# Performance work log

Measured on AMD Instinct MI355X. Metric: run time of the kernel, lower is better.

## Reference

```python
import jax, jax.numpy as jnp
import numpy as np

N_NODES = 50000
N_EDGES = 800000
HIDDEN = 128
EPS = 1e-5


def _layernorm(x, g, b):
    m = jnp.mean(x, axis=-1, keepdims=True)
    v = jnp.var(x, axis=-1, keepdims=True)
    return (x - m) / jnp.sqrt(v + EPS) * g + b


def _batchnorm(x, g, b):
    # training-mode BatchNorm1d: stats over the node (batch) axis, biased var
    m = jnp.mean(x, axis=0, keepdims=True)
    v = jnp.var(x, axis=0, keepdims=True)
    return (x - m) / jnp.sqrt(v + EPS) * g + b


def _instnorm(x):
    # torch InstanceNorm1d on a 2D [N,C] input: unbatched (C,L) view ->
    # normalize each row over the feature axis, no affine params
    m = jnp.mean(x, axis=-1, keepdims=True)
    v = jnp.var(x, axis=-1, keepdims=True)
    return (x - m) / jnp.sqrt(v + EPS)


def _gcn_conv(x, W, b, row, col, norm, n):
    # PyG GCNConv: out[col] += norm * (x @ W)[row]; + bias
    xw = x @ W
    msgs = xw[row] * norm[:, None]          # [E+N, H]
    out = jax.ops.segment_sum(msgs, col, num_segments=n)
    return out + b


def setup_inputs() -> dict:
    key = jax.random.key(0)
    ks = jax.random.split(key, 12)
    H = HIDDEN
    x = jax.random.normal(ks[0], (N_NODES, 2), dtype=jnp.float32)
    edge_index = jax.random.randint(ks[1], (2, N_EDGES), 0, N_NODES, dtype=jnp.int64)

    def lin(k, fan_in, shape):
        bound = 1.0 / np.sqrt(fan_in)
        return jax.random.uniform(k, shape, jnp.float32, -bound, bound)

    inp = {
        "x": x,
        "edge_index": edge_index,
        "coord_W": lin(ks[2], 2, (2, H)),
        "coord_b": lin(ks[3], 2, (H,)),
        "ln_g": jnp.ones((H,), jnp.float32),
        "ln_b": jnp.zeros((H,), jnp.float32),
        "bn_g": jnp.ones((H,), jnp.float32),
        "bn_b": jnp.zeros((H,), jnp.float32),
        "W1": lin(ks[4], H, (H, H)),
        "b1": jnp.zeros((H,), jnp.float32),
        "W2": lin(ks[5], H, (H, H)),
        "b2": jnp.zeros((H,), jnp.float32),
        "W3": lin(ks[6], H, (H, H)),
        "b3": jnp.zeros((H,), jnp.float32),
        "fc1_W": lin(ks[7], H, (H, 32)),
        "fc1_b": lin(ks[8], H, (32,)),
        "fc2_W": lin(ks[9], 32, (32, 2)),
        "fc2_b": lin(ks[10], 32, (2,)),
    }
    return inp


def reference(x, edge_index, coord_W, coord_b, ln_g, ln_b, bn_g, bn_b,
              W1, b1, W2, b2, W3, b3, fc1_W, fc1_b, fc2_W, fc2_b):
    n = x.shape[0]
    loop = jnp.arange(n, dtype=edge_index.dtype)
    row = jnp.concatenate([edge_index[0], loop])
    col = jnp.concatenate([edge_index[1], loop])
    deg = jax.ops.segment_sum(jnp.ones_like(col, dtype=x.dtype), col, num_segments=n)
    dinv = 1.0 / jnp.sqrt(deg)              # deg >= 1 thanks to self-loops
    norm = dinv[row] * dinv[col]

    h = jax.nn.relu(x @ coord_W + coord_b)
    h = _layernorm(h, ln_g, ln_b)

    for W, b in ((W1, b1), (W2, b2), (W3, b3)):
        identity = h
        h = jax.nn.relu(_gcn_conv(h, W, b, row, col, norm, n))
        h = _batchnorm(h, bn_g, bn_b)
        h = _instnorm(h + identity)

    h = jax.nn.relu(h @ fc1_W + fc1_b)
    return jnp.tanh(h @ fc2_W + fc2_b)
```

## Files before the change

### kernel.cpp

```cpp
#include <hip/hip_runtime.h>
#include <hip/hip_bf16.h>
#include <hip/hip_fp16.h>
#include <stdint.h>

#define NN 50000
#define NE 800000
#define HD 128
#define EPSN 1e-5f
#define CAP 1152000

typedef __hip_bfloat16 bf16;
typedef __attribute__((ext_vector_type(8))) _Float16 half8;
typedef __attribute__((ext_vector_type(4))) float f32x4;

__device__ __forceinline__ float us2f(unsigned short u) { return __uint_as_float((uint32_t)u << 16); }
__device__ __forceinline__ ushort f2us(float f) {
    bf16 b = __float2bfloat16(f);
    return *reinterpret_cast<ushort*>(&b);
}
__device__ __forceinline__ ushort f2h(float f) {
    __half h = __float2half(f);
    return *reinterpret_cast<ushort*>(&h);
}
__device__ __forceinline__ float h2f(ushort u) {
    __half h = *reinterpret_cast<__half*>(&u);
    return __half2float(h);
}

__device__ __forceinline__ void cvt8(float4 v, float* o) {
    uint32_t a = __float_as_uint(v.x), b = __float_as_uint(v.y);
    uint32_t c = __float_as_uint(v.z), d = __float_as_uint(v.w);
    o[0] = h2f((ushort)(a & 0xffff)); o[1] = h2f((ushort)(a >> 16));
    o[2] = h2f((ushort)(b & 0xffff)); o[3] = h2f((ushort)(b >> 16));
    o[4] = h2f((ushort)(c & 0xffff)); o[5] = h2f((ushort)(c >> 16));
    o[6] = h2f((ushort)(d & 0xffff)); o[7] = h2f((ushort)(d >> 16));
}

#define O_X    0
#define O_CW   100000
#define O_CB   100256
#define O_LNG  100384
#define O_LNB  100512
#define O_BNG  100640
#define O_BNB  100768
#define O_W1   100896
#define O_B1   117280
#define O_W2   117408
#define O_B2   133792
#define O_W3   133920
#define O_B3   150304
#define O_F1W  150432
#define O_F1B  154528
#define O_F2W  154560
#define O_F2B  154624
#define O_TOT  154626

struct Ptrs { const void* p[17]; };

__device__ const int SEG_OFF[18] = {O_X, O_CW, O_CB, O_LNG, O_LNB, O_BNG, O_BNB,
                                    O_W1, O_B1, O_W2, O_B2, O_W3, O_B3,
                                    O_F1W, O_F1B, O_F2W, O_F2B, O_TOT};

__device__ __forceinline__ int eidx(const int* __restrict__ ei, int isL, int which, int e) {
    size_t base = (size_t)which * NE + e;
    return isL ? ei[2 * base] : ei[base];
}

__global__ void k_detect(const int* __restrict__ ei, const ushort* __restrict__ cw,
                         int* __restrict__ flags) {
    int t = threadIdx.x;
    int v = ei[2 * t + 1] | ei[1000000 + 2 * t + 1];
    int bad = 0;
    if (t < 128) {
        float val = us2f(cw[2 * t]);
        bad = !(fabsf(val) <= 1.0f);
    }
    for (int o = 32; o; o >>= 1) { v |= __shfl_xor(v, o); bad |= __shfl_xor(bad, o); }
    __shared__ int sv[4], sb[4];
    if ((t & 63) == 0) { sv[t >> 6] = v; sb[t >> 6] = bad; }
    __syncthreads();
    if (t == 0) {
        flags[0] = ((sv[0] | sv[1] | sv[2] | sv[3]) == 0) ? 1 : 0;
        flags[1] = ((sb[0] | sb[1] | sb[2] | sb[3]) == 0) ? 1 : 0;
    }
}

__global__ void k_conv(Ptrs ptrs, const int* __restrict__ flags, float* __restrict__ cp,
                       _Float16* __restrict__ wt, int* __restrict__ degR,
                       float* __restrict__ stats, int* __restrict__ cursor,
                       ushort* __restrict__ t0h) {
    int i = blockIdx.x * 256 + threadIdx.x;
    int isBf = flags[1];
    if (i < O_TOT) {
        int s = 0;
        while (i >= SEG_OFF[s + 1]) s++;
        int local = i - SEG_OFF[s];
        const void* src = ptrs.p[s];
        cp[i] = isBf ? us2f(((const ushort*)src)[local]) : ((const float*)src)[local];
    }
    if (i < 3 * HD * HD) {
        int mat = i >> 14, idx = i & (HD * HD - 1);
        int k = idx >> 7, n = idx & 127;
        const void* src = ptrs.p[7 + 2 * mat];
        int local = k * HD + n;
        float v = isBf ? us2f(((const ushort*)src)[local]) : ((const float*)src)[local];
        wt[mat * HD * HD + n * HD + k] = (_Float16)v;
    }
    if (i < 8 * NN) degR[i] = (i < NN) ? 1 : 0;
    if (i < 12288) stats[i] = 0.f;
    if (i < HD) t0h[(size_t)NN * HD + i] = 0;
    if (i == 0) *cursor = 0;
}

__global__ void k_deg(const int* __restrict__ ei, const int* __restrict__ flags,
                      int* __restrict__ degR) {
    int e = blockIdx.x * 256 + threadIdx.x;
    if (e < NE) atomicAdd(&degR[(blockIdx.x & 7) * NN + eidx(ei, flags[0], 1, e)], 1);
}

__global__ void k_fill(const int* __restrict__ ei, const int* __restrict__ flags,
                       int* __restrict__ curA8, int* __restrict__ srw) {
    int e = blockIdx.x * 256 + threadIdx.x;
    if (e >= NE) return;
    int isL = flags[0];
    int r = eidx(ei, isL, 0, e);
    int c = eidx(ei, isL, 1, e);
    int p = atomicAdd(&curA8[(blockIdx.x & 7) * NN + c], 1);
    srw[p] = r << 4;
}


__global__ void k_embed(const float* __restrict__ cp, ushort* __restrict__ h,
                        const int* __restrict__ degR, float* __restrict__ dinv,
                        int* __restrict__ startA, int* __restrict__ curA8,
                        int* __restrict__ cursor, int* __restrict__ srw,
                        int* __restrict__ degO) {
    int gi = blockIdx.x * 256 + threadIdx.x;
    if (gi < NN) {
        int c[8];
        int d = 0;
#pragma unroll
        for (int r = 0; r < 8; r++) { c[r] = degR[r * NN + gi]; d += c[r]; }
        c[0] -= 1;
        degO[gi] = d;
        dinv[gi] = rsqrtf((float)d);
        int cnt = d - 1;
        int cpad = (cnt + 7) & ~7;
        int s = atomicAdd(cursor, cpad);
        startA[gi] = s;
        int off = 0;
#pragma unroll
        for (int r = 0; r < 8; r++) { curA8[r * NN + gi] = s + off; off += c[r]; }
        for (int p = s + cnt; p < s + cpad; p++) srw[p] = NN << 4;
    }
    int node = gi >> 6;
    int lane = threadIdx.x & 63;
    if (node >= NN) return;
    const float* X = cp + O_X;
    const float* CW = cp + O_CW;
    const float* CB = cp + O_CB;
    const float* LG = cp + O_LNG;
    const float* LB = cp + O_LNB;
    float x0 = X[node * 2], x1 = X[node * 2 + 1];
    int f0 = lane, f1 = lane + 64;
    float v0 = fmaxf(0.f, x0 * CW[f0] + x1 * CW[HD + f0] + CB[f0]);
    float v1 = fmaxf(0.f, x0 * CW[f1] + x1 * CW[HD + f1] + CB[f1]);
    float s = v0 + v1, q = v0 * v0 + v1 * v1;
    for (int o = 32; o; o >>= 1) { s += __shfl_xor(s, o); q += __shfl_xor(q, o); }
    float m = s * (1.f / HD);
    float var = q * (1.f / HD) - m * m;
    float r = rsqrtf(var + EPSN);
    h[(size_t)node * HD + f0] = f2h((v0 - m) * r * LG[f0] + LB[f0]);
    h[(size_t)node * HD + f1] = f2h((v1 - m) * r * LG[f1] + LB[f1]);
}


__device__ __forceinline__ void mfma_tile(const _Float16* hl, const _Float16* __restrict__ wt,
                                          const float* __restrict__ dinv,
                                          ushort* __restrict__ t0h, int nodeBase, int t) {
    int w = t >> 6, l = t & 63;
    int m16 = l & 15;
    int kg = l >> 4;
    int node0 = w * 16;
    half8 a[4];
#pragma unroll
    for (int kc = 0; kc < 4; kc++) {
        int nd = node0 + m16;
        int c16 = kc * 4 + kg;
        int chunk = nd * 16 + (c16 ^ (nd & 7));
        a[kc] = *(const half8*)(hl + chunk * 8);
    }
    f32x4 acc[8];
#pragma unroll
    for (int nt = 0; nt < 8; nt++) acc[nt] = (f32x4){0.f, 0.f, 0.f, 0.f};
#pragma unroll
    for (int nt = 0; nt < 8; nt++) {
        const half8* bp = (const half8*)(wt + (size_t)(nt * 16 + m16) * HD);
#pragma unroll
        for (int kc = 0; kc < 4; kc++) {
            acc[nt] = __builtin_amdgcn_mfma_f32_16x16x32_f16(a[kc], bp[kc * 4 + kg],
                                                             acc[nt], 0, 0, 0);
        }
    }
    int ndb = nodeBase + node0 + kg * 4;
#pragma unroll
    for (int rr = 0; rr < 4; rr++) {
        int nd = ndb + rr;
        if (nd < NN) {
            float dv = dinv[nd];
#pragma unroll
            for (int nt = 0; nt < 8; nt++) {
                t0h[(size_t)nd * HD + nt * 16 + m16] = f2h(acc[nt][rr] * dv);
            }
        }
    }
}


__global__ __launch_bounds__(256) void k_gemm(const ushort* __restrict__ h,
                                              const _Float16* __restrict__ wt,
                                              const float* __restrict__ dinv,
                                              ushort* __restrict__ t0h) {
    __shared__ _Float16 hl[64 * HD];
    int t = threadIdx.x;
    int nodeBase = blockIdx.x * 64;
    const uint4* h4 = (const uint4*)h;
#pragma unroll
    for (int r = 0; r < 4; r++) {
        int cid = r * 256 + t;
        int node = cid >> 4;
        int c16 = cid & 15;
        int n = nodeBase + node;
        uint4 v = make_uint4(0u, 0u, 0u, 0u);
        if (n < NN) v = h4[(size_t)n * 16 + c16];
        int chunk = node * 16 + (c16 ^ (node & 7));
        *(uint4*)(hl + chunk * 8) = v;
    }
    __syncthreads();
    mfma_tile(hl, wt, dinv, t0h, nodeBase, t);
}


__global__ __launch_bounds__(256) void k_gemm_fused(const float* __restrict__ agg,
                                                    const float* __restrict__ stats,
                                                    const float* __restrict__ bias,
                                                    const float* __restrict__ bng,
                                                    const float* __restrict__ bnb,
                                                    ushort* __restrict__ h,
                                                    const _Float16* __restrict__ wt,
                                                    const float* __restrict__ dinv,
                                                    ushort* __restrict__ t0h) {
    __shared__ _Float16 hl[64 * HD];
    __shared__ float scL[HD], shL[HD], bL[HD];
    int t = threadIdx.x;
    if (t < 128) {
        const float invN = 1.f / NN;
        float sv = 0.f, qv = 0.f;
#pragma unroll
        for (int r = 0; r < 16; r++) { sv += stats[r * 256 + t]; qv += stats[r * 256 + 128 + t]; }
        float m = sv * invN;
        float v = qv * invN - m * m;
        float sc = bng[t] * rsqrtf(v + EPSN);
        scL[t] = sc;
        shL[t] = bnb[t] - m * sc;
        bL[t] = bias[t];
    }
    __syncthreads();
    int nodeBase = blockIdx.x * 64;
    const float4* a4 = (const float4*)agg;
    const ushort4* h4r = (const ushort4*)h;
    ushort4* h4w = (ushort4*)h;
#pragma unroll
    for (int r = 0; r < 8; r++) {
        int idx = r * 256 + t;
        int node = idx >> 5;
        int c4 = idx & 31;
        int n = nodeBase + node;
        float4 u = make_float4(0.f, 0.f, 0.f, 0.f);
        if (n < NN) {
            float4 av = a4[(size_t)n * 32 + c4];
            ushort4 hv = h4r[(size_t)n * 32 + c4];
            int f = c4 * 4;
            float y0 = fmaxf(0.f, av.x + bL[f]);
            float y1 = fmaxf(0.f, av.y + bL[f + 1]);
            float y2 = fmaxf(0.f, av.z + bL[f + 2]);
            float y3 = fmaxf(0.f, av.w + bL[f + 3]);
            u.x = y0 * scL[f]     + shL[f]     + h2f(hv.x);
            u.y = y1 * scL[f + 1] + shL[f + 1] + h2f(hv.y);
            u.z = y2 * scL[f + 2] + shL[f + 2] + h2f(hv.z);
            u.w = y3 * scL[f + 3] + shL[f + 3] + h2f(hv.w);
        }
        float s = u.x + u.y + u.z + u.w;
        float q = u.x * u.x + u.y * u.y + u.z * u.z + u.w * u.w;
        for (int o = 16; o; o >>= 1) { s += __shfl_xor(s, o); q += __shfl_xor(q, o); }
        float m = s * (1.f / HD);
        float var = q * (1.f / HD) - m * m;
        float rr = rsqrtf(var + EPSN);
        u.x = (u.x - m) * rr; u.y = (u.y - m) * rr;
        u.z = (u.z - m) * rr; u.w = (u.w - m) * rr;
        ushort4 pk;
        pk.x = f2h(u.x); pk.y = f2h(u.y); pk.z = f2h(u.z); pk.w = f2h(u.w);
        if (n < NN) h4w[(size_t)n * 32 + c4] = pk;
        int chunk = node * 16 + ((c4 >> 1) ^ (node & 7));
        *(ushort4*)((char*)hl + chunk * 16 + (c4 & 1) * 8) = pk;
    }
    __syncthreads();
    mfma_tile(hl, wt, dinv, t0h, nodeBase, t);
}


__global__ __launch_bounds__(256) void k_agg(const ushort* __restrict__ t0h,
                                             const int* __restrict__ srw,
                                             const int* __restrict__ startA,
                                             const int* __restrict__ deg,
                                             const float* __restrict__ dinv,
                                             const float* __restrict__ bias,
                                             float* __restrict__ agg,
                                             float* __restrict__ stats) {
    int t = threadIdx.x;
    int w = t >> 6;
    int l = t & 63;
    int g = l >> 4;
    int k = l & 15;
    int l32 = l & 31;
    const float4* t04 = (const float4*)t0h;
    float4* agg4 = (float4*)agg;
    float bs[8];
    {
        const float4* b4 = (const float4*)bias;
        float4 u0 = b4[2 * k], u1 = b4[2 * k + 1];
        bs[0] = u0.x; bs[1] = u0.y; bs[2] = u0.z; bs[3] = u0.w;
        bs[4] = u1.x; bs[5] = u1.y; bs[6] = u1.z; bs[7] = u1.w;
    }
    float rs1[8], rs2[8];
#pragma unroll
    for (int m = 0; m < 8; m++) { rs1[m] = 0.f; rs2[m] = 0.f; }
    int stride = gridDim.x * 4;
    int i = blockIdx.x * 4 + w;
    int s = 0, nb = 0;
    float di = 0.f;
    if (i < NN) {
        s = startA[i];
        nb = (deg[i] - 1 + 7) & ~7;
        di = dinv[i];
    }
    while (i < NN) {
        float4 sv = t04[(size_t)i * 16 + k];
        int ex = 0;
        if (l32 < nb) ex = srw[s + l32];
        int nb4 = nb >> 2;
        float4 gg[8];
#define GATH(b) { int rv = __shfl(ex, 4 * (b) + g); \
                  gg[b] = t04[(size_t)(uint32_t)rv + k]; }
        if (nb4 > 0) { GATH(0) GATH(1) }
        if (nb4 > 2) { GATH(2) GATH(3) }
        if (nb4 > 4) { GATH(4) GATH(5) }
        if (nb4 > 6) { GATH(6) GATH(7) }
#undef GATH
        int inext = i + stride;
        int sN = 0, nbN = 0;
        float diN = 0.f;
        if (inext < NN) {
            sN = startA[inext];
            nbN = (deg[inext] - 1 + 7) & ~7;
            diN = dinv[inext];
        }
        float acc[8], c8[8];
        cvt8(sv, c8);
        float ws = (g == 0) ? 1.f : 0.f;
#pragma unroll
        for (int m = 0; m < 8; m++) acc[m] = ws * c8[m];
#define ACCB(b) { float d8[8]; cvt8(gg[b], d8); \
                  _Pragma("unroll") \
                  for (int m = 0; m < 8; m++) acc[m] += d8[m]; }
        if (nb4 > 0) { ACCB(0) ACCB(1) }
        if (nb4 > 2) { ACCB(2) ACCB(3) }
        if (nb4 > 4) { ACCB(4) ACCB(5) }
        if (nb4 > 6) { ACCB(6) ACCB(7) }
#undef ACCB
        for (int j = 32; j < nb; j += 32) {
            int ex2 = 0;
            if (j + l32 < nb) ex2 = srw[s + j + l32];
            int rem4 = (nb - j) >> 2;
            if (rem4 > 8) rem4 = 8;
            for (int b = 0; b < rem4; b += 2) {
                int r0 = __shfl(ex2, 4 * b + g);
                int r1 = __shfl(ex2, 4 * b + 4 + g);
                float4 g0 = t04[(size_t)(uint32_t)r0 + k];
                float4 g1 = t04[(size_t)(uint32_t)r1 + k];
                float d0[8], d1[8];
                cvt8(g0, d0); cvt8(g1, d1);
#pragma unroll
                for (int m = 0; m < 8; m++) acc[m] += d0[m] + d1[m];
            }
        }
#pragma unroll
        for (int m = 0; m < 8; m++) {
            acc[m] += __shfl_xor(acc[m], 16);
            acc[m] += __shfl_xor(acc[m], 32);
            acc[m] *= di;
        }
        if (g == 0) {
            agg4[(size_t)i * 32 + 2 * k]     = make_float4(acc[0], acc[1], acc[2], acc[3]);
            agg4[(size_t)i * 32 + 2 * k + 1] = make_float4(acc[4], acc[5], acc[6], acc[7]);
        }
#pragma unroll
        for (int m = 0; m < 8; m++) {
            float y = fmaxf(0.f, acc[m] + bs[m]);
            rs1[m] += y;
            rs2[m] += y * y;
        }
        i = inext; s = sN; nb = nbN; di = diN;
    }
    __shared__ float s1[4][HD], s2[4][HD];
    if (l < 16) {
#pragma unroll
        for (int m = 0; m < 8; m++) {
            s1[w][k * 8 + m] = rs1[m];
            s2[w][k * 8 + m] = rs2[m];
        }
    }
    __syncthreads();
    float* st = stats + (blockIdx.x & 15) * 256;
    if (t < 128) {
        atomicAdd(&st[t], s1[0][t] + s1[1][t] + s1[2][t] + s1[3][t]);
    } else {
        int f = t - 128;
        atomicAdd(&st[128 + f], s2[0][f] + s2[1][f] + s2[2][f] + s2[3][f]);
    }
}


__global__ __launch_bounds__(256) void k_tail(const float* __restrict__ agg,
                                              const float* __restrict__ stats,
                                              const ushort* __restrict__ h,
                                              const float* __restrict__ cp,
                                              const int* __restrict__ flags,
                                              void* __restrict__ outv) {
    __shared__ float W1l[HD * 32];
    __shared__ float ub[4][HD];
    __shared__ float scT[HD], shT[HD], bT[HD];
    __shared__ float B1s[32], W2s[64], B2s[2];
    int t = threadIdx.x;
    const float4* f1w4 = (const float4*)(cp + O_F1W);
    float4* w14 = (float4*)W1l;
#pragma unroll
    for (int r = 0; r < 4; r++) w14[r * 256 + t] = f1w4[r * 256 + t];
    if (t < 32) B1s[t] = cp[O_F1B + t];
    if (t < 64) W2s[t] = cp[O_F2W + t];
    if (t < 2) B2s[t] = cp[O_F2B + t];
    if (t < 128) {
        const float invN = 1.f / NN;
        float sv = 0.f, qv = 0.f;
#pragma unroll
        for (int r = 0; r < 16; r++) { sv += stats[r * 256 + t]; qv += stats[r * 256 + 128 + t]; }
        float m = sv * invN;
        float v = qv * invN - m * m;
        float sc = cp[O_BNG + t] * rsqrtf(v + EPSN);
        scT[t] = sc;
        shT[t] = cp[O_BNB + t] - m * sc;
        bT[t] = cp[O_B3 + t];
    }
    __syncthreads();
    int isBf = flags[1];
    int w = t >> 6, l = t & 63;
    int f = l & 31, half = l >> 5;
    for (int base = blockIdx.x * 4; base < NN; base += gridDim.x * 4) {
        int node = base + w;
        if (node >= NN) continue;
        size_t o = (size_t)node * HD;
        float a0 = agg[o + l], a1 = agg[o + l + 64];
        float h0 = h2f(h[o + l]), h1 = h2f(h[o + l + 64]);
        float y0 = fmaxf(0.f, a0 + bT[l]);
        float y1 = fmaxf(0.f, a1 + bT[l + 64]);
        float u0 = y0 * scT[l]      + shT[l]      + h0;
        float u1 = y1 * scT[l + 64] + shT[l + 64] + h1;
        float s = u0 + u1, q = u0 * u0 + u1 * u1;
        for (int oo = 32; oo; oo >>= 1) { s += __shfl_xor(s, oo); q += __shfl_xor(q, oo); }
        float m = s * (1.f / HD);
        float var = q * (1.f / HD) - m * m;
        float r = rsqrtf(var + EPSN);
        u0 = (u0 - m) * r; u1 = (u1 - m) * r;
        ub[w][l] = u0; ub[w][l + 64] = u1;
        float acc = (half == 0) ? B1s[f] : 0.f;
        const float* up = ub[w] + half * 64;
        const float* wp = W1l + half * 64 * 32 + f;
#pragma unroll 16
        for (int kk = 0; kk < 64; kk++) acc += up[kk] * wp[kk * 32];
        acc += __shfl_xor(acc, 32);
        float av = fmaxf(0.f, acc);
        float p0 = av * W2s[f * 2], p1 = av * W2s[f * 2 + 1];
        for (int oo = 16; oo; oo >>= 1) { p0 += __shfl_xor(p0, oo); p1 += __shfl_xor(p1, oo); }
        if (l == 0) {
            p0 = tanhf(p0 + B2s[0]); p1 = tanhf(p1 + B2s[1]);
            if (isBf) {
                ((uint32_t*)outv)[node] = (uint32_t)f2us(p0) | ((uint32_t)f2us(p1) << 16);
            } else {
                float2 ov; ov.x = p0; ov.y = p1;
                ((float2*)outv)[node] = ov;
            }
        }
    }
}


extern "C" void kernel_launch(void* const* d_in, const int* in_sizes, int n_in,
                              void* d_out, int out_size, void* d_ws, size_t ws_size,
                              hipStream_t stream) {
    const int* ei = (const int*)d_in[1];

    Ptrs ptrs;
    ptrs.p[0] = d_in[0];
    for (int s = 1; s < 17; s++) ptrs.p[s] = d_in[s + 1];

    char* wsp = (char*)d_ws;
    size_t off = 0;
    auto alloc = [&](size_t bytes) {
        void* p = wsp + off;
        off += (bytes + 255) & ~(size_t)255;
        return p;
    };
    float* cp     = (float*)alloc((size_t)O_TOT * 4);
    ushort* h     = (ushort*)alloc((size_t)NN * HD * 2);
    ushort* t0h   = (ushort*)alloc((size_t)(NN + 1) * HD * 2);
    float* agg    = (float*)alloc((size_t)NN * HD * 4);
    int* degR     = (int*)alloc((size_t)8 * NN * 4);
    int* degO     = (int*)alloc((size_t)NN * 4);
    float* dinv   = (float*)alloc((size_t)NN * 4);
    int* srw      = (int*)alloc((size_t)CAP * 4);
    int* startA   = (int*)alloc((size_t)NN * 4);
    int* curA8    = (int*)alloc((size_t)8 * NN * 4);
    float* stats  = (float*)alloc(3 * 4096 * 4);
    int* cursor   = (int*)alloc(256);
    int* flags    = (int*)alloc(256);
    _Float16* wt  = (_Float16*)alloc((size_t)3 * HD * HD * 2);

    const int BN_EDGE = (NE + 255) / 256;
    const int BN_CONV = (8 * NN + 255) / 256;
    const int BN_GEMM = (NN + 63) / 64;

    const float* B[3] = {cp + O_B1, cp + O_B2, cp + O_B3};

    k_detect<<<1, 256, 0, stream>>>(ei, (const ushort*)d_in[2], flags);
    k_conv<<<BN_CONV, 256, 0, stream>>>(ptrs, flags, cp, wt, degR, stats, cursor, t0h);
    k_deg<<<BN_EDGE, 256, 0, stream>>>(ei, flags, degR);
    k_embed<<<NN / 4, 256, 0, stream>>>(cp, h, degR, dinv, startA, curA8, cursor, srw, degO);
    k_fill<<<BN_EDGE, 256, 0, stream>>>(ei, flags, curA8, srw);

    k_gemm<<<BN_GEMM, 256, 0, stream>>>(h, wt, dinv, t0h);
    k_agg<<<2048, 256, 0, stream>>>(t0h, srw, startA, degO, dinv, B[0], agg, stats);
    for (int l = 1; l < 3; l++) {
        k_gemm_fused<<<BN_GEMM, 256, 0, stream>>>(agg, stats + 4096 * (l - 1),
                                                  B[l - 1], cp + O_BNG, cp + O_BNB,
                                                  h, wt + (size_t)l * HD * HD, dinv, t0h);
        k_agg<<<2048, 256, 0, stream>>>(t0h, srw, startA, degO, dinv, B[l],
                                        agg, stats + 4096 * l);
    }
    k_tail<<<2048, 256, 0, stream>>>(agg, stats + 8192, h, cp, flags, d_out);
}
```

Before: 414.5 us.

## Build CSR via class-partitioned two-pass scatter with prefix-scan node offsets

Replaces the atomic cursor allocation of per-node edge segments with a deterministic two-level prefix scan, so neighbour lists are laid out in node order. Edges are first bucketed into 49 destination-node classes of 1024 nodes, then each class is scattered by a single block so the per-node atomics and srw writes hit a localized region. This aims to improve locality for both CSR construction and the later aggregation reads. It adds several small kernels, including a single-block serial scan, plus an extra 8-byte-per-edge intermediate buffer and pass.

```diff
diff --git a/kernel.cpp b/kernel.cpp
--- a/kernel.cpp
+++ b/kernel.cpp
@@ -8,6 +8,8 @@
 #define HD 128
 #define EPSN 1e-5f
 #define CAP 1152000
+#define NCLS 49
+#define NSB 196
 
 typedef __hip_bfloat16 bf16;
 typedef __attribute__((ext_vector_type(8))) _Float16 half8;
@@ -87,7 +89,7 @@
 
 __global__ void k_conv(Ptrs ptrs, const int* __restrict__ flags, float* __restrict__ cp,
                        _Float16* __restrict__ wt, int* __restrict__ degR,
-                       float* __restrict__ stats, int* __restrict__ cursor,
+                       int* __restrict__ ccR, float* __restrict__ stats,
                        ushort* __restrict__ t0h) {
     int i = blockIdx.x * 256 + threadIdx.x;
     int isBf = flags[1];
@@ -107,50 +109,131 @@
         wt[mat * HD * HD + n * HD + k] = (_Float16)v;
     }
     if (i < 8 * NN) degR[i] = (i < NN) ? 1 : 0;
+    if (i < 32 * NCLS) ccR[i] = 0;
     if (i < 12288) stats[i] = 0.f;
     if (i < HD) t0h[(size_t)NN * HD + i] = 0;
-    if (i == 0) *cursor = 0;
-}
-
-__global__ void k_deg(const int* __restrict__ ei, const int* __restrict__ flags,
-                      int* __restrict__ degR) {
-    int e = blockIdx.x * 256 + threadIdx.x;
-    if (e < NE) atomicAdd(&degR[(blockIdx.x & 7) * NN + eidx(ei, flags[0], 1, e)], 1);
-}
-
-__global__ void k_fill(const int* __restrict__ ei, const int* __restrict__ flags,
-                       int* __restrict__ curA8, int* __restrict__ srw) {
+}
+
+__global__ __launch_bounds__(256) void k_count(const int* __restrict__ ei,
+                                               const int* __restrict__ flags,
+                                               int* __restrict__ degR,
+                                               int* __restrict__ ccR) {
+    __shared__ int lcc[NCLS];
+    int t = threadIdx.x;
+    if (t < NCLS) lcc[t] = 0;
+    __syncthreads();
+    int e = blockIdx.x * 256 + t;
+    if (e < NE) {
+        int c = eidx(ei, flags[0], 1, e);
+        atomicAdd(&degR[(blockIdx.x & 7) * NN + c], 1);
+        atomicAdd(&lcc[c >> 10], 1);
+    }
+    __syncthreads();
+    if (t < NCLS && lcc[t] > 0)
+        atomicAdd(&ccR[(blockIdx.x & 31) * NCLS + t], lcc[t]);
+}
+
+__global__ __launch_bounds__(256) void k_scan1(const int* __restrict__ degR,
+                                               int* __restrict__ degO,
+                                               float* __restrict__ dinv,
+                                               int* __restrict__ nodePref,
+                                               int* __restrict__ blockSum) {
+    __shared__ int lp[256];
+    int i = blockIdx.x * 256 + threadIdx.x;
+    int cpad = 0;
+    if (i < NN) {
+        int d = 0;
+#pragma unroll
+        for (int r = 0; r < 8; r++) d += degR[r * NN + i];
+        degO[i] = d;
+        dinv[i] = rsqrtf((float)d);
+        cpad = (d - 1 + 7) & ~7;
+    }
+    lp[threadIdx.x] = cpad;
+    __syncthreads();
+    if (threadIdx.x == 0) {
+        int run = 0;
+        for (int t = 0; t < 256; t++) { int v = lp[t]; lp[t] = run; run += v; }
+        blockSum[blockIdx.x] = run;
+    }
+    __syncthreads();
+    if (i < NN) nodePref[i] = lp[threadIdx.x];
+}
+
+__global__ __launch_bounds__(256) void k_scan2(int* __restrict__ blockSum,
+                                               const int* __restrict__ ccR,
+                                               int* __restrict__ cur2,
+                                               int* __restrict__ classBase) {
+    __shared__ int sB[NSB], sC[32 * NCLS], tot[NCLS], cb[NCLS + 1];
+    int t = threadIdx.x;
+    if (t < NSB) sB[t] = blockSum[t];
+    for (int j = t; j < 32 * NCLS; j += 256) sC[j] = ccR[j];
+    __syncthreads();
+    if (t < NCLS) {
+        int s = 0;
+        for (int r = 0; r < 32; r++) s += sC[r * NCLS + t];
+        tot[t] = s;
+    }
+    if (t == 64) {
+        int run = 0;
+        for (int b = 0; b < NSB; b++) { int v = sB[b]; sB[b] = run; run += v; }
+    }
+    __syncthreads();
+    if (t == 0) {
+        int run = 0;
+        for (int c = 0; c < NCLS; c++) { cb[c] = run; run += tot[c]; }
+        cb[NCLS] = run;
+    }
+    __syncthreads();
+    if (t < NCLS) {
+        int base = cb[t];
+        for (int r = 0; r < 32; r++) { int v = sC[r * NCLS + t]; sC[r * NCLS + t] = base; base += v; }
+        classBase[t] = cb[t];
+        if (t == 0) classBase[NCLS] = cb[NCLS];
+    }
+    __syncthreads();
+    if (t < NSB) blockSum[t] = sB[t];
+    for (int j = t; j < 32 * NCLS; j += 256) cur2[j] = sC[j];
+}
+
+__global__ __launch_bounds__(256) void k_part(const int* __restrict__ ei,
+                                              const int* __restrict__ flags,
+                                              int* __restrict__ cur2,
+                                              int2* __restrict__ part) {
     int e = blockIdx.x * 256 + threadIdx.x;
     if (e >= NE) return;
     int isL = flags[0];
     int r = eidx(ei, isL, 0, e);
     int c = eidx(ei, isL, 1, e);
-    int p = atomicAdd(&curA8[(blockIdx.x & 7) * NN + c], 1);
-    srw[p] = r << 4;
+    int p = atomicAdd(&cur2[(blockIdx.x & 31) * NCLS + (c >> 10)], 1);
+    part[p] = make_int2(r << 4, c);
+}
+
+__global__ __launch_bounds__(1024) void k_scatter(const int2* __restrict__ part,
+                                                  const int* __restrict__ classBase,
+                                                  int* __restrict__ curA,
+                                                  int* __restrict__ srw) {
+    int cls = blockIdx.x;
+    int lo = classBase[cls], hi = classBase[cls + 1];
+    for (int idx = lo + threadIdx.x; idx < hi; idx += 1024) {
+        int2 e = part[idx];
+        int p = atomicAdd(&curA[e.y], 1);
+        srw[p] = e.x;
+    }
 }
 
 
 __global__ void k_embed(const float* __restrict__ cp, ushort* __restrict__ h,
-                        const int* __restrict__ degR, float* __restrict__ dinv,
-                        int* __restrict__ startA, int* __restrict__ curA8,
-                        int* __restrict__ cursor, int* __restrict__ srw,
-                        int* __restrict__ degO) {
+                        const int* __restrict__ degO, const int* __restrict__ nodePref,
+                        const int* __restrict__ blockSum, int* __restrict__ startA,
+                        int* __restrict__ curA, int* __restrict__ srw) {
     int gi = blockIdx.x * 256 + threadIdx.x;
     if (gi < NN) {
-        int c[8];
-        int d = 0;
-#pragma unroll
-        for (int r = 0; r < 8; r++) { c[r] = degR[r * NN + gi]; d += c[r]; }
-        c[0] -= 1;
-        degO[gi] = d;
-        dinv[gi] = rsqrtf((float)d);
-        int cnt = d - 1;
+        int s = blockSum[gi >> 8] + nodePref[gi];
+        startA[gi] = s;
+        curA[gi] = s;
+        int cnt = degO[gi] - 1;
         int cpad = (cnt + 7) & ~7;
-        int s = atomicAdd(cursor, cpad);
-        startA[gi] = s;
-        int off = 0;
-#pragma unroll
-        for (int r = 0; r < 8; r++) { curA8[r * NN + gi] = s + off; off += c[r]; }
         for (int p = s + cnt; p < s + cpad; p++) srw[p] = NN << 4;
     }
     int node = gi >> 6;
@@ -528,10 +611,15 @@
     int* degO     = (int*)alloc((size_t)NN * 4);
     float* dinv   = (float*)alloc((size_t)NN * 4);
     int* srw      = (int*)alloc((size_t)CAP * 4);
+    int2* part    = (int2*)alloc((size_t)NE * 8);
     int* startA   = (int*)alloc((size_t)NN * 4);
-    int* curA8    = (int*)alloc((size_t)8 * NN * 4);
+    int* curA     = (int*)alloc((size_t)NN * 4);
+    int* nodePref = (int*)alloc((size_t)NN * 4);
+    int* blockSum = (int*)alloc((size_t)NSB * 4);
+    int* classBase= (int*)alloc((size_t)(NCLS + 1) * 4);
+    int* ccR      = (int*)alloc((size_t)32 * NCLS * 4);
+    int* cur2     = (int*)alloc((size_t)32 * NCLS * 4);
     float* stats  = (float*)alloc(3 * 4096 * 4);
-    int* cursor   = (int*)alloc(256);
     int* flags    = (int*)alloc(256);
     _Float16* wt  = (_Float16*)alloc((size_t)3 * HD * HD * 2);
 
@@ -542,10 +630,13 @@
     const float* B[3] = {cp + O_B1, cp + O_B2, cp + O_B3};
 
     k_detect<<<1, 256, 0, stream>>>(ei, (const ushort*)d_in[2], flags);
-    k_conv<<<BN_CONV, 256, 0, stream>>>(ptrs, flags, cp, wt, degR, stats, cursor, t0h);
-    k_deg<<<BN_EDGE, 256, 0, stream>>>(ei, flags, degR);
-    k_embed<<<NN / 4, 256, 0, stream>>>(cp, h, degR, dinv, startA, curA8, cursor, srw, degO);
-    k_fill<<<BN_EDGE, 256, 0, stream>>>(ei, flags, curA8, srw);
+    k_conv<<<BN_CONV, 256, 0, stream>>>(ptrs, flags, cp, wt, degR, ccR, stats, t0h);
+    k_count<<<BN_EDGE, 256, 0, stream>>>(ei, flags, degR, ccR);
+    k_scan1<<<NSB, 256, 0, stream>>>(degR, degO, dinv, nodePref, blockSum);
+    k_scan2<<<1, 256, 0, stream>>>(blockSum, ccR, cur2, classBase);
+    k_embed<<<NN / 4, 256, 0, stream>>>(cp, h, degO, nodePref, blockSum, startA, curA, srw);
+    k_part<<<BN_EDGE, 256, 0, stream>>>(ei, flags, cur2, part);
+    k_scatter<<<NCLS, 1024, 0, stream>>>(part, classBase, curA, srw);
 
     k_gemm<<<BN_GEMM, 256, 0, stream>>>(h, wt, dinv, t0h);
     k_agg<<<2048, 256, 0, stream>>>(t0h, srw, startA, degO, dinv, B[0], agg, stats);
```

Result: slower. 496.7 us (+19.8%).
